# Kernel optimization log

Hardware: AMD Instinct MI355X
Metric: run time of the kernel (lower is better)

The kernel has to match this reference:

```python
import jax, jax.numpy as jnp
import numpy as np

B, T, E, H, M2 = 8, 2048, 256, 2, 134
HD = E // H


def setup_inputs() -> dict:
    key = jax.random.key(0)
    ks = jax.random.split(key, 10)
    s = 0.02
    return {
        "X": jax.random.normal(ks[0], (B, T, E), dtype=jnp.float32),
        "Y": jax.random.uniform(ks[1], (B, M2), dtype=jnp.float32),
        "wpe": s * jax.random.normal(ks[2], (T, E), dtype=jnp.float32),
        "ln1_g": jnp.ones((E,), jnp.float32), "ln1_b": jnp.zeros((E,), jnp.float32),
        "attn_w": s * jax.random.normal(ks[3], (3 * E, E), dtype=jnp.float32),
        "attn_b": jnp.zeros((3 * E,), jnp.float32),
        "attnproj_w": s * jax.random.normal(ks[4], (E, E), dtype=jnp.float32),
        "attnproj_b": jnp.zeros((E,), jnp.float32),
        "ln2_g": jnp.ones((E,), jnp.float32), "ln2_b": jnp.zeros((E,), jnp.float32),
        "fc_w": s * jax.random.normal(ks[5], (2 * E, E), dtype=jnp.float32),
        "fc_b": jnp.zeros((2 * E,), jnp.float32),
        "mlpproj_w": s * jax.random.normal(ks[6], (E, 2 * E), dtype=jnp.float32),
        "mlpproj_b": jnp.zeros((E,), jnp.float32),
        "lnf_g": jnp.ones((E,), jnp.float32), "lnf_b": jnp.zeros((E,), jnp.float32),
        "head_w": s * jax.random.normal(ks[7], (M2, E), dtype=jnp.float32),
        "head_b": jnp.zeros((M2,), jnp.float32),
    }


def _ln(x, g, b, eps=1e-5):
    mu = x.mean(-1, keepdims=True)
    var = ((x - mu) ** 2).mean(-1, keepdims=True)
    return (x - mu) * jax.lax.rsqrt(var + eps) * g + b


def reference(X, Y, wpe, ln1_g, ln1_b, attn_w, attn_b, attnproj_w, attnproj_b,
              ln2_g, ln2_b, fc_w, fc_b, mlpproj_w, mlpproj_b, lnf_g, lnf_b,
              head_w, head_b):
    # positional ids = arange(T) -> wpe itself; cls ids = [0]*T/2 + [1]*T/2
    cls_ids = np.concatenate([np.zeros(T // 2, np.int32), np.ones(T // 2, np.int32)])
    x = X + wpe + wpe[cls_ids]                      # [B,T,E] (dropout = identity, eval)

    # single Block (n_layer=1), preceded by ReLU as in cross_mod loop
    x = jax.nn.relu(x)
    h = _ln(x, ln1_g, ln1_b)
    qkv = h @ attn_w.T + attn_b                     # [B,T,3E]
    q, k, v = jnp.split(qkv, 3, axis=-1)
    q, k, v = jax.nn.relu(q), jax.nn.relu(k), jax.nn.relu(v)
    split_heads = lambda t: t.reshape(B, T, H, HD).transpose(0, 2, 1, 3)
    q, k, v = split_heads(q), split_heads(k), split_heads(v)
    att = jnp.einsum('bhqd,bhkd->bhqk', q, k) * (1.0 / np.sqrt(HD))
    tril = jnp.tril(jnp.ones((T, T), dtype=bool))
    # masked_fill(-inf) then ReLU  ==  zero outside causal mask, ReLU inside
    att = jnp.where(tril, jax.nn.relu(att), 0.0)    # [B,H,T,T]
    y = jnp.einsum('bhqk,bhkd->bhqd', att, v)
    y = y.transpose(0, 2, 1, 3).reshape(B, T, E)
    x = x + (y @ attnproj_w.T + attnproj_b)

    h = _ln(x, ln2_g, ln2_b)
    x = x + (jax.nn.relu(h @ fc_w.T + fc_b) @ mlpproj_w.T + mlpproj_b)

    x = jax.nn.relu(x)
    x = _ln(x, lnf_g, lnf_b)
    x = jax.nn.relu(x)
    emb = x.mean(axis=1)                            # [B,E]
    logits = jax.nn.relu(emb @ head_w.T + head_b)   # [B,M2]

    loss1 = jnp.sqrt(jnp.mean((logits - Y) ** 2))
    e1, e2 = emb[:, : E // 2], emb[:, E // 2:]
    loss3 = jnp.sqrt(jnp.mean((e1 - e2) ** 2))
    loss = 50.0 * loss1 + loss3
    return (e1, e2, loss, loss1, loss3, logits)
```

## Files before the change

kernel.cpp:

```cpp
#include <hip/hip_runtime.h>
#include <hip/hip_bf16.h>

#define Bc 8
#define Tc 2048
#define Ec 256
#define Hc 2
#define HDc 128
#define Mrows (Bc*Tc)
#define M2c 134

using bfx8  = __attribute__((ext_vector_type(8))) __bf16;
using f32x4 = __attribute__((ext_vector_type(4))) float;

__device__ __forceinline__ void gll16(const __bf16* g, __bf16* lds) {
    __builtin_amdgcn_global_load_lds(
        (const __attribute__((address_space(1))) unsigned int*)g,
        (__attribute__((address_space(3))) unsigned int*)lds, 16, 0, 0);
}

__global__ __launch_bounds__(256) void embed_prep_k(const float* X, const float* wpe,
                                                    const float* g, const float* bb,
                                                    const float* attn_w, const float* apw,
                                                    const float* fcw, const float* mpw,
                                                    __bf16* wb, float* embsum,
                                                    __bf16* xres, __bf16* hb) {
    int m = blockIdx.x;
    int e = threadIdx.x;
    if (m < 2048) {
        int i = m * 256 + e;
        if (i < 196608)       wb[i] = (__bf16)attn_w[i];
        else if (i < 262144)  wb[i] = (__bf16)apw[i - 196608];
        else if (i < 393216)  wb[i] = (__bf16)fcw[i - 262144];
        else                  wb[i] = (__bf16)mpw[i - 393216];
        if (m < 8) embsum[m * 256 + e] = 0.f;
    }
    int t = m & (Tc - 1);
    float v = X[(size_t)m * Ec + e] + wpe[(size_t)t * Ec + e] + wpe[(size_t)(t >= 1024) * Ec + e];
    v = fmaxf(v, 0.f);
    xres[(size_t)m * Ec + e] = (__bf16)v;
    float s1 = v, s2 = v * v;
    #pragma unroll
    for (int o = 32; o; o >>= 1) { s1 += __shfl_xor(s1, o, 64); s2 += __shfl_xor(s2, o, 64); }
    __shared__ float a1[4], a2[4];
    int w = threadIdx.x >> 6;
    if ((threadIdx.x & 63) == 0) { a1[w] = s1; a2[w] = s2; }
    __syncthreads();
    float m1 = (a1[0] + a1[1] + a1[2] + a1[3]) * (1.f / 256.f);
    float m2 = (a2[0] + a2[1] + a2[2] + a2[3]) * (1.f / 256.f);
    float r = rsqrtf(m2 - m1 * m1 + 1e-5f);
    hb[(size_t)m * Ec + e] = (__bf16)((v - m1) * r * g[e] + bb[e]);
}

__global__ __launch_bounds__(256) void gemm_qkv(const __bf16* __restrict__ A,
                                                const __bf16* __restrict__ Bw,
                                                const float* __restrict__ bias,
                                                __bf16* __restrict__ Qb,
                                                __bf16* __restrict__ Kb,
                                                __bf16* __restrict__ Vb) {
    const int K = 256;
    __shared__ __bf16 As[128 * 64];
    __shared__ __bf16 Bs[128 * 64];
    const int tid = threadIdx.x, w = tid >> 6, l = tid & 63;
    const int m0 = blockIdx.y * 128, n0 = blockIdx.x * 128;
    const int wr = w >> 1, wc = w & 1;
    const int quad = l >> 4, col15 = l & 15;

    f32x4 acc[4][4];
    f32x4 zz = {0.f, 0.f, 0.f, 0.f};
    #pragma unroll
    for (int i = 0; i < 4; i++)
        #pragma unroll
        for (int j = 0; j < 4; j++) acc[i][j] = zz;

    const int lrow = l >> 3;
    const int pbs  = l & 7;

    for (int kb = 0; kb < K; kb += 64) {
        #pragma unroll
        for (int it = 0; it < 4; it++) {
            int chunk = w * 4 + it;
            int row = chunk * 8 + lrow;
            int lb = pbs ^ (row & 7);
            gll16(A  + (size_t)(m0 + row) * K + kb + lb * 8, As + chunk * 512);
            gll16(Bw + (size_t)(n0 + row) * K + kb + lb * 8, Bs + chunk * 512);
        }
        __syncthreads();
        #pragma unroll
        for (int ks = 0; ks < 2; ks++) {
            bfx8 af[4], bfr[4];
            #pragma unroll
            for (int rt = 0; rt < 4; rt++) {
                int row = wr * 64 + rt * 16 + col15;
                int pb = (ks * 4 + quad) ^ (row & 7);
                af[rt] = *(const bfx8*)(As + row * 64 + pb * 8);
            }
            #pragma unroll
            for (int ct = 0; ct < 4; ct++) {
                int row = wc * 64 + ct * 16 + col15;
                int pb = (ks * 4 + quad) ^ (row & 7);
                bfr[ct] = *(const bfx8*)(Bs + row * 64 + pb * 8);
            }
            #pragma unroll
            for (int rt = 0; rt < 4; rt++)
                #pragma unroll
                for (int ct = 0; ct < 4; ct++)
                    acc[rt][ct] = __builtin_amdgcn_mfma_f32_16x16x32_bf16(af[rt], bfr[ct], acc[rt][ct], 0, 0, 0);
        }
        __syncthreads();
    }

    #pragma unroll
    for (int rt = 0; rt < 4; rt++)
        #pragma unroll
        for (int ct = 0; ct < 4; ct++) {
            int mgb = m0 + wr * 64 + rt * 16 + quad * 4;
            int ng  = n0 + wc * 64 + ct * 16 + col15;
            float bsv = bias[ng];
            #pragma unroll
            for (int r = 0; r < 4; r++) {
                float val = fmaxf(acc[rt][ct][r] + bsv, 0.f);
                int mg = mgb + r;
                int sel = ng >> 8;
                int hh = (ng >> 7) & 1;
                int d = ng & 127;
                int bb = mg >> 11, tt = mg & (Tc - 1);
                size_t idx = ((size_t)((bb * 2 + hh) * Tc + tt)) * HDc + d;
                __bf16 bv = (__bf16)val;
                if (sel == 0) Qb[idx] = bv;
                else if (sel == 1) Kb[idx] = bv;
                else Vb[idx] = bv;
            }
        }
}

__global__ __launch_bounds__(256) void transpose_v(const unsigned short* Vb, unsigned short* Vt) {
    __shared__ unsigned short tile[64][66];
    int kt = blockIdx.x, dt = blockIdx.y, bh = blockIdx.z;
    int tid = threadIdx.x;
    int k0 = kt * 64, d0 = dt * 64;
    int rr = tid >> 4, cc = (tid & 15) * 4;
    #pragma unroll
    for (int p = 0; p < 4; p++) {
        int k = p * 16 + rr;
        const unsigned short* src = Vb + ((size_t)(bh * Tc + k0 + k)) * HDc + d0 + cc;
        ushort4 vv = *(const ushort4*)src;
        tile[k][cc] = vv.x; tile[k][cc + 1] = vv.y; tile[k][cc + 2] = vv.z; tile[k][cc + 3] = vv.w;
    }
    __syncthreads();
    #pragma unroll
    for (int p = 0; p < 4; p++) {
        int d = p * 16 + rr;
        unsigned short* dst = Vt + ((size_t)(bh * HDc + d0 + d)) * Tc + k0 + cc;
        ushort4 ov;
        ov.x = tile[cc][d]; ov.y = tile[cc + 1][d]; ov.z = tile[cc + 2][d]; ov.w = tile[cc + 3][d];
        *(ushort4*)dst = ov;
    }
}

__global__ __launch_bounds__(256, 4) void attn6_k(const __bf16* __restrict__ Qb,
                                                  const __bf16* __restrict__ Kb,
                                                  const __bf16* __restrict__ Vt,
                                                  __bf16* __restrict__ Y1,
                                                  __bf16* __restrict__ Y2,
                                                  __bf16* __restrict__ Y3,
                                                  __bf16* __restrict__ Y4) {
    __shared__ __bf16 Ks[64 * 128];
    __shared__ __bf16 Vs[128 * 64];
    __shared__ __bf16 Ss[64 * 64];
    int bid = blockIdx.x;
    int lane8 = bid & 7;
    int s = bid >> 3;
    int bh = ((s & 1) << 3) | lane8;
    int f = s >> 1;
    int qt, ch;
    if (f < 8)       { qt = f;                    ch = 0; }
    else if (f < 24) { qt = 8 + ((f - 8) >> 1);   ch = (f - 8) & 1; }
    else if (f < 48) { int r = f - 24; int d3 = r / 3; qt = 16 + d3; ch = r - 3 * d3; }
    else             { int r = f - 48; qt = 24 + (r >> 2); ch = r & 3; }
    int Q0 = qt * 64;
    int kts = ch * 8;
    int kte = min(kts + 8, qt + 1);

    int tid = threadIdx.x, w = tid >> 6, l = tid & 63;
    int quad = l >> 4, col15 = l & 15;
    const int lrowK = l >> 4, pbsK = l & 15;
    const int lrowV = l >> 3, pbsV = l & 7;

    #pragma unroll
    for (int it = 0; it < 4; it++) {
        int chunk = w * 4 + it;
        int row = chunk * 4 + lrowK;
        int lb = pbsK ^ (row & 7);
        gll16(Qb + ((size_t)(bh * Tc + Q0 + row)) * HDc + lb * 8, Ks + chunk * 512);
    }
    __syncthreads();
    bfx8 qf[4];
    #pragma unroll
    for (int ks = 0; ks < 4; ks++) {
        int row = w * 16 + col15;
        int pb = (ks * 4 + quad) ^ (row & 7);
        qf[ks] = *(const bfx8*)(Ks + row * 128 + pb * 8);
    }

    f32x4 zz = {0.f, 0.f, 0.f, 0.f};
    f32x4 yacc[8];
    #pragma unroll
    for (int i = 0; i < 8; i++) yacc[i] = zz;

    for (int kt = kts; kt < kte; kt++) {
        __syncthreads();
        #pragma unroll
        for (int it = 0; it < 4; it++) {
            int chunk = w * 4 + it;
            int rowK = chunk * 4 + lrowK;
            int lbK = pbsK ^ (rowK & 7);
            gll16(Kb + ((size_t)(bh * Tc + kt * 64 + rowK)) * HDc + lbK * 8, Ks + chunk * 512);
            int rowV = chunk * 8 + lrowV;
            int lbV = pbsV ^ (rowV & 7);
            gll16(Vt + ((size_t)(bh * HDc + rowV)) * Tc + kt * 64 + lbV * 8, Vs + chunk * 512);
        }
        __syncthreads();

        f32x4 sacc[4];
        #pragma unroll
        for (int i = 0; i < 4; i++) sacc[i] = zz;
        #pragma unroll
        for (int ks = 0; ks < 4; ks++) {
            #pragma unroll
            for (int ct = 0; ct < 4; ct++) {
                int row = ct * 16 + col15;
                int pb = (ks * 4 + quad) ^ (row & 7);
                bfx8 kf = *(const bfx8*)(Ks + row * 128 + pb * 8);
                sacc[ct] = __builtin_amdgcn_mfma_f32_16x16x32_bf16(qf[ks], kf, sacc[ct], 0, 0, 0);
            }
        }

        #pragma unroll
        for (int ct = 0; ct < 4; ct++) {
            int kl = ct * 16 + col15;
            int kg = kt * 64 + kl;
            int blk = kl >> 3, off = kl & 7;
            #pragma unroll
            for (int r = 0; r < 4; r++) {
                int qlw = w * 16 + quad * 4 + r;
                float val = (kg <= Q0 + qlw) ? fmaxf(sacc[ct][r], 0.f) : 0.f;
                int pb = blk ^ (qlw & 7);
                Ss[qlw * 64 + pb * 8 + off] = (__bf16)val;
            }
        }

        #pragma unroll
        for (int ks = 0; ks < 2; ks++) {
            int rowS = w * 16 + col15;
            int pbS = (ks * 4 + quad) ^ (rowS & 7);
            bfx8 sf = *(const bfx8*)(Ss + rowS * 64 + pbS * 8);
            #pragma unroll
            for (int dt = 0; dt < 8; dt++) {
                int row = dt * 16 + col15;
                int pb = (ks * 4 + quad) ^ (row & 7);
                bfx8 vf = *(const bfx8*)(Vs + row * 64 + pb * 8);
                yacc[dt] = __builtin_amdgcn_mfma_f32_16x16x32_bf16(sf, vf, yacc[dt], 0, 0, 0);
            }
        }
    }

    __bf16* Yp = (ch == 0) ? Y1 : (ch == 1) ? Y2 : (ch == 2) ? Y3 : Y4;
    int b = bh >> 1, h = bh & 1;
    const float sc = 0.08838834764831845f;
    #pragma unroll
    for (int dt = 0; dt < 8; dt++) {
        int d = dt * 16 + col15;
        #pragma unroll
        for (int r = 0; r < 4; r++) {
            int q = Q0 + w * 16 + quad * 4 + r;
            Yp[((size_t)(b * Tc + q)) * Ec + h * HDc + d] = (__bf16)(yacc[dt][r] * sc);
        }
    }
}

__global__ __launch_bounds__(256, 1) void mega_k(const __bf16* __restrict__ Y1,
                                                 const __bf16* __restrict__ Y2,
                                                 const __bf16* __restrict__ Y3,
                                                 const __bf16* __restrict__ Y4,
                                                 const __bf16* __restrict__ wap,
                                                 const float* __restrict__ apb,
                                                 const __bf16* __restrict__ xres,
                                                 const float* __restrict__ ln2_g,
                                                 const float* __restrict__ ln2_b,
                                                 const __bf16* __restrict__ wfc,
                                                 const float* __restrict__ fcb,
                                                 const __bf16* __restrict__ wmp,
                                                 const float* __restrict__ mpb,
                                                 const float* __restrict__ lnf_g,
                                                 const float* __restrict__ lnf_b,
                                                 float* __restrict__ embsum) {
    __shared__ __bf16 h2s[4 * 4096];
    __shared__ __bf16 fc64[8 * 4096];
    __shared__ __bf16 Bs[256 * 64];
    __shared__ float cs[256];
    const int tid = threadIdx.x, w = tid >> 6, l = tid & 63;
    const int m0 = blockIdx.x * 64;
    const int quad = l >> 4, col15 = l & 15;
    const int lrow = l >> 3, pbs = l & 7;
    f32x4 zz = {0.f, 0.f, 0.f, 0.f};
    cs[tid] = 0.f;

    int nsum = (((m0 & (Tc - 1)) >> 6) + 8) >> 3;
    const __bf16* Ys[4] = {Y1, Y2, Y3, Y4};
    __bf16* As = fc64;

    f32x4 acc[16];
    #pragma unroll
    for (int i = 0; i < 16; i++) acc[i] = zz;

    for (int kb = 0; kb < 256; kb += 64) {
        bfx8 av[2]; int rows[2], blks[2];
        #pragma unroll
        for (int it = 0; it < 2; it++) {
            int idx = it * 256 + tid;
            int row = idx >> 3, blk = idx & 7;
            rows[it] = row; blks[it] = blk;
            size_t off = (size_t)(m0 + row) * 256 + kb + blk * 8;
            bfx8 a1 = *(const bfx8*)(Y1 + off);
            float tmp[8];
            #pragma unroll
            for (int jj = 0; jj < 8; jj++) tmp[jj] = (float)a1[jj];
            for (int j = 1; j < nsum; j++) {
                bfx8 aj = *(const bfx8*)(Ys[j] + off);
                #pragma unroll
                for (int jj = 0; jj < 8; jj++) tmp[jj] += (float)aj[jj];
            }
            #pragma unroll
            for (int jj = 0; jj < 8; jj++) a1[jj] = (__bf16)tmp[jj];
            av[it] = a1;
        }
        __syncthreads();
        #pragma unroll
        for (int it = 0; it < 2; it++) {
            int row = rows[it];
            int pb = blks[it] ^ (row & 7);
            *(bfx8*)(As + row * 64 + pb * 8) = av[it];
        }
        #pragma unroll
        for (int it = 0; it < 8; it++) {
            int chunk = w * 8 + it;
            int row = chunk * 8 + lrow;
            int lb = pbs ^ (row & 7);
            gll16(wap + (size_t)row * 256 + kb + lb * 8, Bs + chunk * 512);
        }
        __syncthreads();
        #pragma unroll
        for (int ks = 0; ks < 2; ks++) {
            int arow = w * 16 + col15;
            int apbk = (ks * 4 + quad) ^ (arow & 7);
            bfx8 af = *(const bfx8*)(As + arow * 64 + apbk * 8);
            #pragma unroll
            for (int ct = 0; ct < 16; ct++) {
                int brow = ct * 16 + col15;
                int bpb = (ks * 4 + quad) ^ (brow & 7);
                bfx8 bf = *(const bfx8*)(Bs + brow * 64 + bpb * 8);
                acc[ct] = __builtin_amdgcn_mfma_f32_16x16x32_bf16(af, bf, acc[ct], 0, 0, 0);
            }
        }
    }

    float xv[16][4];
    #pragma unroll
    for (int ct = 0; ct < 16; ct++) {
        int ng = ct * 16 + col15;
        float bsv = apb[ng];
        #pragma unroll
        for (int r = 0; r < 4; r++) {
            int mg = m0 + w * 16 + quad * 4 + r;
            xv[ct][r] = acc[ct][r] + bsv + (float)xres[(size_t)mg * 256 + ng];
        }
    }
    {
        float s1[4], s2[4];
        #pragma unroll
        for (int r = 0; r < 4; r++) {
            float a = 0.f, b2 = 0.f;
            #pragma unroll
            for (int ct = 0; ct < 16; ct++) { a += xv[ct][r]; b2 += xv[ct][r] * xv[ct][r]; }
            #pragma unroll
            for (int o = 1; o < 16; o <<= 1) { a += __shfl_xor(a, o, 64); b2 += __shfl_xor(b2, o, 64); }
            s1[r] = a; s2[r] = b2;
        }
        #pragma unroll
        for (int r = 0; r < 4; r++) {
            float mu = s1[r] * (1.f / 256.f);
            float var = s2[r] * (1.f / 256.f) - mu * mu;
            float rs = rsqrtf(var + 1e-5f);
            int row = w * 16 + quad * 4 + r;
            #pragma unroll
            for (int ct = 0; ct < 16; ct++) {
                int ng = ct * 16 + col15;
                float h = (xv[ct][r] - mu) * rs * ln2_g[ng] + ln2_b[ng];
                int panel = ng >> 6, c = ng & 63;
                h2s[panel * 4096 + row * 64 + ((c >> 3) ^ (row & 7)) * 8 + (c & 7)] = (__bf16)h;
            }
        }
    }

    for (int half = 0; half < 2; half++) {
        f32x4 acc2[16];
        #pragma unroll
        for (int i = 0; i < 16; i++) acc2[i] = zz;
        for (int kb = 0; kb < 256; kb += 64) {
            __syncthreads();
            #pragma unroll
            for (int it = 0; it < 8; it++) {
                int chunk = w * 8 + it;
                int row = chunk * 8 + lrow;
                int lb = pbs ^ (row & 7);
                gll16(wfc + (size_t)(half * 256 + row) * 256 + kb + lb * 8, Bs + chunk * 512);
            }
            __syncthreads();
            int panel = kb >> 6;
            #pragma unroll
            for (int ks = 0; ks < 2; ks++) {
                int arow = w * 16 + col15;
                int apbk = (ks * 4 + quad) ^ (arow & 7);
                bfx8 af = *(const bfx8*)(h2s + panel * 4096 + arow * 64 + apbk * 8);
                #pragma unroll
                for (int ct = 0; ct < 16; ct++) {
                    int brow = ct * 16 + col15;
                    int bpb = (ks * 4 + quad) ^ (brow & 7);
                    bfx8 bf = *(const bfx8*)(Bs + brow * 64 + bpb * 8);
                    acc2[ct] = __builtin_amdgcn_mfma_f32_16x16x32_bf16(af, bf, acc2[ct], 0, 0, 0);
                }
            }
        }
        #pragma unroll
        for (int ct = 0; ct < 16; ct++) {
            int col = half * 256 + ct * 16 + col15;
            float bsv = fcb[col];
            int panel = col >> 6, c = col & 63;
            #pragma unroll
            for (int r = 0; r < 4; r++) {
                int row = w * 16 + quad * 4 + r;
                float val = fmaxf(acc2[ct][r] + bsv, 0.f);
                fc64[panel * 4096 + row * 64 + ((c >> 3) ^ (row & 7)) * 8 + (c & 7)] = (__bf16)val;
            }
        }
    }

    #pragma unroll
    for (int i = 0; i < 16; i++) acc[i] = zz;
    for (int kb = 0; kb < 512; kb += 64) {
        __syncthreads();
        #pragma unroll
        for (int it = 0; it < 8; it++) {
            int chunk = w * 8 + it;
            int row = chunk * 8 + lrow;
            int lb = pbs ^ (row & 7);
            gll16(wmp + (size_t)row * 512 + kb + lb * 8, Bs + chunk * 512);
        }
        __syncthreads();
        int panel = kb >> 6;
        #pragma unroll
        for (int ks = 0; ks < 2; ks++) {
            int arow = w * 16 + col15;
            int apbk = (ks * 4 + quad) ^ (arow & 7);
            bfx8 af = *(const bfx8*)(fc64 + panel * 4096 + arow * 64 + apbk * 8);
            #pragma unroll
            for (int ct = 0; ct < 16; ct++) {
                int brow = ct * 16 + col15;
                int bpb = (ks * 4 + quad) ^ (brow & 7);
                bfx8 bf = *(const bfx8*)(Bs + brow * 64 + bpb * 8);
                acc[ct] = __builtin_amdgcn_mfma_f32_16x16x32_bf16(af, bf, acc[ct], 0, 0, 0);
            }
        }
    }

    #pragma unroll
    for (int ct = 0; ct < 16; ct++) {
        int ng = ct * 16 + col15;
        float bsv = mpb[ng];
        #pragma unroll
        for (int r = 0; r < 4; r++)
            xv[ct][r] = fmaxf(acc[ct][r] + bsv + xv[ct][r], 0.f);
    }
    float s1[4], s2[4];
    #pragma unroll
    for (int r = 0; r < 4; r++) {
        float a = 0.f, b2 = 0.f;
        #pragma unroll
        for (int ct = 0; ct < 16; ct++) { a += xv[ct][r]; b2 += xv[ct][r] * xv[ct][r]; }
        #pragma unroll
        for (int o = 1; o < 16; o <<= 1) { a += __shfl_xor(a, o, 64); b2 += __shfl_xor(b2, o, 64); }
        s1[r] = a; s2[r] = b2;
    }
    float colsum[16];
    #pragma unroll
    for (int ct = 0; ct < 16; ct++) colsum[ct] = 0.f;
    #pragma unroll
    for (int r = 0; r < 4; r++) {
        float mu = s1[r] * (1.f / 256.f);
        float var = s2[r] * (1.f / 256.f) - mu * mu;
        float rs = rsqrtf(var + 1e-5f);
        #pragma unroll
        for (int ct = 0; ct < 16; ct++) {
            int ng = ct * 16 + col15;
            float h = (xv[ct][r] - mu) * rs * lnf_g[ng] + lnf_b[ng];
            colsum[ct] += fmaxf(h, 0.f);
        }
    }
    #pragma unroll
    for (int ct = 0; ct < 16; ct++) {
        colsum[ct] += __shfl_xor(colsum[ct], 16, 64);
        colsum[ct] += __shfl_xor(colsum[ct], 32, 64);
    }
    if (quad == 0) {
        #pragma unroll
        for (int ct = 0; ct < 16; ct++)
            atomicAdd(&cs[ct * 16 + col15], colsum[ct]);
    }
    __syncthreads();
    atomicAdd(&embsum[(m0 >> 11) * 256 + tid], cs[tid]);
}

__global__ __launch_bounds__(256) void final_k(const float* embsum, const float* Yt,
                                               const float* head_w, const float* head_b,
                                               float* out) {
    __shared__ float semb[2048];
    __shared__ float slog[1072];
    int tid = threadIdx.x;
    for (int i = tid; i < 2048; i += 256) semb[i] = embsum[i] * (1.f / 2048.f);
    __syncthreads();
    float part1 = 0.f;
    for (int idx = tid; idx < 1072; idx += 256) {
        int b = idx / M2c, n = idx - b * M2c;
        float acc = head_b[n];
        const float* wn = head_w + (size_t)n * Ec;
        const float* e = semb + b * Ec;
        #pragma unroll 8
        for (int k = 0; k < Ec; k++) acc += e[k] * wn[k];
        acc = fmaxf(acc, 0.f);
        slog[idx] = acc;
        float d = acc - Yt[idx];
        part1 += d * d;
    }
    float part3 = 0.f;
    for (int idx = tid; idx < 1024; idx += 256) {
        int b = idx >> 7, i = idx & 127;
        float d = semb[b * Ec + i] - semb[b * Ec + 128 + i];
        part3 += d * d;
    }
    #pragma unroll
    for (int o = 32; o; o >>= 1) { part1 += __shfl_xor(part1, o, 64); part3 += __shfl_xor(part3, o, 64); }
    __shared__ float r1[4], r3[4];
    int w = tid >> 6;
    if ((tid & 63) == 0) { r1[w] = part1; r3[w] = part3; }
    __syncthreads();
    float l1 = sqrtf((r1[0] + r1[1] + r1[2] + r1[3]) / 1072.f);
    float l3 = sqrtf((r3[0] + r3[1] + r3[2] + r3[3]) / 1024.f);
    for (int idx = tid; idx < 1024; idx += 256) {
        int b = idx >> 7, i = idx & 127;
        out[idx]        = semb[b * Ec + i];
        out[1024 + idx] = semb[b * Ec + 128 + i];
    }
    if (tid == 0) {
        out[2048] = 50.f * l1 + l3;
        out[2049] = l1;
        out[2050] = l3;
    }
    for (int idx = tid; idx < 1072; idx += 256) out[2051 + idx] = slog[idx];
}

extern "C" void kernel_launch(void* const* d_in, const int* in_sizes, int n_in,
                              void* d_out, int out_size, void* d_ws, size_t ws_size,
                              hipStream_t stream) {
    const float* X        = (const float*)d_in[0];
    const float* Yt       = (const float*)d_in[1];
    const float* wpe      = (const float*)d_in[2];
    const float* ln1_g    = (const float*)d_in[3];
    const float* ln1_b    = (const float*)d_in[4];
    const float* attn_w   = (const float*)d_in[5];
    const float* attn_b   = (const float*)d_in[6];
    const float* apw      = (const float*)d_in[7];
    const float* apb      = (const float*)d_in[8];
    const float* ln2_g    = (const float*)d_in[9];
    const float* ln2_b    = (const float*)d_in[10];
    const float* fcw      = (const float*)d_in[11];
    const float* fcb      = (const float*)d_in[12];
    const float* mpw      = (const float*)d_in[13];
    const float* mpb      = (const float*)d_in[14];
    const float* lnf_g    = (const float*)d_in[15];
    const float* lnf_b    = (const float*)d_in[16];
    const float* head_w   = (const float*)d_in[17];
    const float* head_b   = (const float*)d_in[18];

    char* ws = (char*)d_ws;
    const size_t MB = 1048576;
    __bf16* xres   = (__bf16*)(ws + 0 * MB);
    __bf16* hb     = (__bf16*)(ws + 8 * MB);
    __bf16* Qb     = (__bf16*)(ws + 16 * MB);
    __bf16* Kb     = (__bf16*)(ws + 24 * MB);
    __bf16* Vb     = (__bf16*)(ws + 32 * MB);
    __bf16* Vt     = (__bf16*)(ws + 40 * MB);
    __bf16* Y1     = (__bf16*)(ws + 48 * MB);
    __bf16* Y2     = (__bf16*)(ws + 56 * MB);
    __bf16* wb     = (__bf16*)(ws + 64 * MB);
    float*  embsum = (float*)(ws + 65 * MB);

    __bf16* Y3 = hb;
    __bf16* Y4 = Vb;

    __bf16* wqkv = wb;
    __bf16* wap  = wb + 196608;
    __bf16* wfc  = wb + 262144;
    __bf16* wmp  = wb + 393216;

    embed_prep_k<<<Mrows, 256, 0, stream>>>(X, wpe, ln1_g, ln1_b,
                                            attn_w, apw, fcw, mpw, wb, embsum, xres, hb);
    gemm_qkv<<<dim3(6, 128), 256, 0, stream>>>(hb, wqkv, attn_b, Qb, Kb, Vb);
    transpose_v<<<dim3(32, 2, 16), 256, 0, stream>>>((const unsigned short*)Vb, (unsigned short*)Vt);
    attn6_k<<<1280, 256, 0, stream>>>(Qb, Kb, Vt, Y1, Y2, Y3, Y4);
    mega_k<<<256, 256, 0, stream>>>(Y1, Y2, Y3, Y4, wap, apb, xres, ln2_g, ln2_b,
                                    wfc, fcb, wmp, mpb, lnf_g, lnf_b, embsum);
    final_k<<<1, 256, 0, stream>>>(embsum, Yt, head_w, head_b, (float*)d_out);
}
```

Baseline: 250.4 us.

## Fuse V transpose into QKV GEMM epilogue and retile MLP mega kernel

The QKV GEMM now writes V tiles straight into the transposed Vt layout through an LDS staging buffer, so the separate transpose_v kernel and its extra round trip through global memory go away. The fused post-attention kernel is retiled from 64 to 32 rows per block, doubling the grid to 512 blocks with two blocks per CU. Each wave now owns a column slice of the output, reads weight fragments directly from global/L2 instead of staging them in LDS, and combines LayerNorm statistics across waves through shared memory. This trades LDS weight reuse for more parallelism, and it raises LDS use in the GEMM plus the number of global weight reads.

```diff
diff --git a/kernel.cpp b/kernel.cpp
--- a/kernel.cpp
+++ b/kernel.cpp
@@ -56,14 +56,16 @@
                                                 const float* __restrict__ bias,
                                                 __bf16* __restrict__ Qb,
                                                 __bf16* __restrict__ Kb,
-                                                __bf16* __restrict__ Vb) {
+                                                unsigned short* __restrict__ Vt) {
     const int K = 256;
     __shared__ __bf16 As[128 * 64];
     __shared__ __bf16 Bs[128 * 64];
+    __shared__ unsigned short trans[128][136];
     const int tid = threadIdx.x, w = tid >> 6, l = tid & 63;
     const int m0 = blockIdx.y * 128, n0 = blockIdx.x * 128;
     const int wr = w >> 1, wc = w & 1;
     const int quad = l >> 4, col15 = l & 15;
+    const int isV = (n0 >= 512);
 
     f32x4 acc[4][4];
     f32x4 zz = {0.f, 0.f, 0.f, 0.f};
@@ -113,47 +115,39 @@
     for (int rt = 0; rt < 4; rt++)
         #pragma unroll
         for (int ct = 0; ct < 4; ct++) {
-            int mgb = m0 + wr * 64 + rt * 16 + quad * 4;
             int ng  = n0 + wc * 64 + ct * 16 + col15;
             float bsv = bias[ng];
             #pragma unroll
             for (int r = 0; r < 4; r++) {
+                int mg = m0 + wr * 64 + rt * 16 + quad * 4 + r;
                 float val = fmaxf(acc[rt][ct][r] + bsv, 0.f);
-                int mg = mgb + r;
-                int sel = ng >> 8;
-                int hh = (ng >> 7) & 1;
-                int d = ng & 127;
-                int bb = mg >> 11, tt = mg & (Tc - 1);
-                size_t idx = ((size_t)((bb * 2 + hh) * Tc + tt)) * HDc + d;
                 __bf16 bv = (__bf16)val;
-                if (sel == 0) Qb[idx] = bv;
-                else if (sel == 1) Kb[idx] = bv;
-                else Vb[idx] = bv;
-            }
-        }
-}
-
-__global__ __launch_bounds__(256) void transpose_v(const unsigned short* Vb, unsigned short* Vt) {
-    __shared__ unsigned short tile[64][66];
-    int kt = blockIdx.x, dt = blockIdx.y, bh = blockIdx.z;
-    int tid = threadIdx.x;
-    int k0 = kt * 64, d0 = dt * 64;
-    int rr = tid >> 4, cc = (tid & 15) * 4;
-    #pragma unroll
-    for (int p = 0; p < 4; p++) {
-        int k = p * 16 + rr;
-        const unsigned short* src = Vb + ((size_t)(bh * Tc + k0 + k)) * HDc + d0 + cc;
-        ushort4 vv = *(const ushort4*)src;
-        tile[k][cc] = vv.x; tile[k][cc + 1] = vv.y; tile[k][cc + 2] = vv.z; tile[k][cc + 3] = vv.w;
-    }
-    __syncthreads();
-    #pragma unroll
-    for (int p = 0; p < 4; p++) {
-        int d = p * 16 + rr;
-        unsigned short* dst = Vt + ((size_t)(bh * HDc + d0 + d)) * Tc + k0 + cc;
-        ushort4 ov;
-        ov.x = tile[cc][d]; ov.y = tile[cc + 1][d]; ov.z = tile[cc + 2][d]; ov.w = tile[cc + 3][d];
-        *(ushort4*)dst = ov;
+                if (isV) {
+                    int d = ng & 127;
+                    int tl = mg - m0;
+                    trans[d][tl] = *(unsigned short*)&bv;
+                } else {
+                    int sel = ng >> 8;
+                    int hh = (ng >> 7) & 1;
+                    int d = ng & 127;
+                    int bb = mg >> 11, tt = mg & (Tc - 1);
+                    size_t idx = ((size_t)((bb * 2 + hh) * Tc + tt)) * HDc + d;
+                    if (sel == 0) Qb[idx] = bv;
+                    else Kb[idx] = bv;
+                }
+            }
+        }
+    if (isV) {
+        __syncthreads();
+        int h = (n0 >> 7) & 1;
+        int b = m0 >> 11, t0 = m0 & (Tc - 1);
+        int bh = b * 2 + h;
+        int d = tid >> 1, th = tid & 1;
+        unsigned short* dst = Vt + ((size_t)(bh * HDc + d)) * Tc + t0 + th * 64;
+        const unsigned short* src = &trans[d][th * 64];
+        #pragma unroll
+        for (int i = 0; i < 8; i++)
+            *(uint4*)(dst + i * 8) = *(const uint4*)(src + i * 8);
     }
 }
 
@@ -278,243 +272,245 @@
     }
 }
 
-__global__ __launch_bounds__(256, 1) void mega_k(const __bf16* __restrict__ Y1,
+__global__ __launch_bounds__(256, 2) void mega_k(const __bf16* __restrict__ Y1,
                                                  const __bf16* __restrict__ Y2,
                                                  const __bf16* __restrict__ Y3,
                                                  const __bf16* __restrict__ Y4,
                                                  const __bf16* __restrict__ wap,
-                                                 const float* __restrict__ apb,
+                                                 const float* __restrict__ apbias,
                                                  const __bf16* __restrict__ xres,
                                                  const float* __restrict__ ln2_g,
                                                  const float* __restrict__ ln2_b,
                                                  const __bf16* __restrict__ wfc,
-                                                 const float* __restrict__ fcb,
+                                                 const float* __restrict__ fcbias,
                                                  const __bf16* __restrict__ wmp,
-                                                 const float* __restrict__ mpb,
+                                                 const float* __restrict__ mpbias,
                                                  const float* __restrict__ lnf_g,
                                                  const float* __restrict__ lnf_b,
                                                  float* __restrict__ embsum) {
-    __shared__ __bf16 h2s[4 * 4096];
-    __shared__ __bf16 fc64[8 * 4096];
-    __shared__ __bf16 Bs[256 * 64];
+    __shared__ __bf16 fcs[32 * 512];
+    __shared__ __bf16 h2s[32 * 256];
+    __shared__ float red1[32][4], red2[32][4];
     __shared__ float cs[256];
+    __bf16* As = fcs;
+
     const int tid = threadIdx.x, w = tid >> 6, l = tid & 63;
-    const int m0 = blockIdx.x * 64;
+    const int m0 = blockIdx.x * 32;
     const int quad = l >> 4, col15 = l & 15;
-    const int lrow = l >> 3, pbs = l & 7;
     f32x4 zz = {0.f, 0.f, 0.f, 0.f};
-    cs[tid] = 0.f;
-
-    int nsum = (((m0 & (Tc - 1)) >> 6) + 8) >> 3;
+
+    int qt = (m0 & (Tc - 1)) >> 6;
+    int nsum = (qt + 8) >> 3;
     const __bf16* Ys[4] = {Y1, Y2, Y3, Y4};
-    __bf16* As = fc64;
-
-    f32x4 acc[16];
-    #pragma unroll
-    for (int i = 0; i < 16; i++) acc[i] = zz;
-
-    for (int kb = 0; kb < 256; kb += 64) {
-        bfx8 av[2]; int rows[2], blks[2];
-        #pragma unroll
-        for (int it = 0; it < 2; it++) {
-            int idx = it * 256 + tid;
-            int row = idx >> 3, blk = idx & 7;
-            rows[it] = row; blks[it] = blk;
-            size_t off = (size_t)(m0 + row) * 256 + kb + blk * 8;
-            bfx8 a1 = *(const bfx8*)(Y1 + off);
-            float tmp[8];
-            #pragma unroll
-            for (int jj = 0; jj < 8; jj++) tmp[jj] = (float)a1[jj];
-            for (int j = 1; j < nsum; j++) {
-                bfx8 aj = *(const bfx8*)(Ys[j] + off);
-                #pragma unroll
-                for (int jj = 0; jj < 8; jj++) tmp[jj] += (float)aj[jj];
-            }
-            #pragma unroll
-            for (int jj = 0; jj < 8; jj++) a1[jj] = (__bf16)tmp[jj];
-            av[it] = a1;
-        }
-        __syncthreads();
-        #pragma unroll
-        for (int it = 0; it < 2; it++) {
-            int row = rows[it];
-            int pb = blks[it] ^ (row & 7);
-            *(bfx8*)(As + row * 64 + pb * 8) = av[it];
-        }
-        #pragma unroll
-        for (int it = 0; it < 8; it++) {
-            int chunk = w * 8 + it;
-            int row = chunk * 8 + lrow;
-            int lb = pbs ^ (row & 7);
-            gll16(wap + (size_t)row * 256 + kb + lb * 8, Bs + chunk * 512);
-        }
-        __syncthreads();
-        #pragma unroll
-        for (int ks = 0; ks < 2; ks++) {
-            int arow = w * 16 + col15;
-            int apbk = (ks * 4 + quad) ^ (arow & 7);
-            bfx8 af = *(const bfx8*)(As + arow * 64 + apbk * 8);
-            #pragma unroll
-            for (int ct = 0; ct < 16; ct++) {
-                int brow = ct * 16 + col15;
-                int bpb = (ks * 4 + quad) ^ (brow & 7);
-                bfx8 bf = *(const bfx8*)(Bs + brow * 64 + bpb * 8);
-                acc[ct] = __builtin_amdgcn_mfma_f32_16x16x32_bf16(af, bf, acc[ct], 0, 0, 0);
-            }
-        }
-    }
-
-    float xv[16][4];
-    #pragma unroll
-    for (int ct = 0; ct < 16; ct++) {
-        int ng = ct * 16 + col15;
-        float bsv = apb[ng];
-        #pragma unroll
-        for (int r = 0; r < 4; r++) {
-            int mg = m0 + w * 16 + quad * 4 + r;
-            xv[ct][r] = acc[ct][r] + bsv + (float)xres[(size_t)mg * 256 + ng];
-        }
-    }
-    {
-        float s1[4], s2[4];
+
+    #pragma unroll
+    for (int it = 0; it < 4; it++) {
+        int idx = it * 256 + tid;
+        int row = idx >> 5, blk = idx & 31;
+        size_t off = (size_t)(m0 + row) * 256 + blk * 8;
+        bfx8 a1 = *(const bfx8*)(Y1 + off);
+        float tmp[8];
+        #pragma unroll
+        for (int jj = 0; jj < 8; jj++) tmp[jj] = (float)a1[jj];
+        for (int j = 1; j < nsum; j++) {
+            bfx8 aj = *(const bfx8*)(Ys[j] + off);
+            #pragma unroll
+            for (int jj = 0; jj < 8; jj++) tmp[jj] += (float)aj[jj];
+        }
+        #pragma unroll
+        for (int jj = 0; jj < 8; jj++) a1[jj] = (__bf16)tmp[jj];
+        *(bfx8*)(As + row * 256 + (blk ^ (row & 7)) * 8) = a1;
+    }
+    __syncthreads();
+
+    f32x4 acc1[2][4];
+    #pragma unroll
+    for (int rt = 0; rt < 2; rt++)
+        #pragma unroll
+        for (int ct = 0; ct < 4; ct++) acc1[rt][ct] = zz;
+    #pragma unroll
+    for (int kw = 0; kw < 8; kw++) {
+        bfx8 af[2], bf[4];
+        #pragma unroll
+        for (int rt = 0; rt < 2; rt++) {
+            int row = rt * 16 + col15;
+            int pb = (kw * 4 + quad) ^ (row & 7);
+            af[rt] = *(const bfx8*)(As + row * 256 + pb * 8);
+        }
+        #pragma unroll
+        for (int ct = 0; ct < 4; ct++)
+            bf[ct] = *(const bfx8*)(wap + (size_t)(w * 64 + ct * 16 + col15) * 256 + kw * 32 + quad * 8);
+        #pragma unroll
+        for (int rt = 0; rt < 2; rt++)
+            #pragma unroll
+            for (int ct = 0; ct < 4; ct++)
+                acc1[rt][ct] = __builtin_amdgcn_mfma_f32_16x16x32_bf16(af[rt], bf[ct], acc1[rt][ct], 0, 0, 0);
+    }
+
+    float xv[2][4][4];
+    #pragma unroll
+    for (int rt = 0; rt < 2; rt++)
+        #pragma unroll
+        for (int ct = 0; ct < 4; ct++) {
+            int ng = w * 64 + ct * 16 + col15;
+            float bsv = apbias[ng];
+            #pragma unroll
+            for (int r = 0; r < 4; r++) {
+                int mg = m0 + rt * 16 + quad * 4 + r;
+                xv[rt][ct][r] = acc1[rt][ct][r] + bsv + (float)xres[(size_t)mg * 256 + ng];
+            }
+        }
+    #pragma unroll
+    for (int rt = 0; rt < 2; rt++)
         #pragma unroll
         for (int r = 0; r < 4; r++) {
             float a = 0.f, b2 = 0.f;
             #pragma unroll
-            for (int ct = 0; ct < 16; ct++) { a += xv[ct][r]; b2 += xv[ct][r] * xv[ct][r]; }
+            for (int ct = 0; ct < 4; ct++) { a += xv[rt][ct][r]; b2 += xv[rt][ct][r] * xv[rt][ct][r]; }
             #pragma unroll
             for (int o = 1; o < 16; o <<= 1) { a += __shfl_xor(a, o, 64); b2 += __shfl_xor(b2, o, 64); }
-            s1[r] = a; s2[r] = b2;
-        }
+            if (col15 == 0) {
+                int row = rt * 16 + quad * 4 + r;
+                red1[row][w] = a; red2[row][w] = b2;
+            }
+        }
+    __syncthreads();
+    #pragma unroll
+    for (int rt = 0; rt < 2; rt++)
         #pragma unroll
         for (int r = 0; r < 4; r++) {
-            float mu = s1[r] * (1.f / 256.f);
-            float var = s2[r] * (1.f / 256.f) - mu * mu;
+            int row = rt * 16 + quad * 4 + r;
+            float s1 = red1[row][0] + red1[row][1] + red1[row][2] + red1[row][3];
+            float s2 = red2[row][0] + red2[row][1] + red2[row][2] + red2[row][3];
+            float mu = s1 * (1.f / 256.f);
+            float var = s2 * (1.f / 256.f) - mu * mu;
             float rs = rsqrtf(var + 1e-5f);
-            int row = w * 16 + quad * 4 + r;
-            #pragma unroll
-            for (int ct = 0; ct < 16; ct++) {
-                int ng = ct * 16 + col15;
-                float h = (xv[ct][r] - mu) * rs * ln2_g[ng] + ln2_b[ng];
-                int panel = ng >> 6, c = ng & 63;
-                h2s[panel * 4096 + row * 64 + ((c >> 3) ^ (row & 7)) * 8 + (c & 7)] = (__bf16)h;
-            }
-        }
-    }
-
-    for (int half = 0; half < 2; half++) {
-        f32x4 acc2[16];
-        #pragma unroll
-        for (int i = 0; i < 16; i++) acc2[i] = zz;
-        for (int kb = 0; kb < 256; kb += 64) {
-            __syncthreads();
-            #pragma unroll
-            for (int it = 0; it < 8; it++) {
-                int chunk = w * 8 + it;
-                int row = chunk * 8 + lrow;
-                int lb = pbs ^ (row & 7);
-                gll16(wfc + (size_t)(half * 256 + row) * 256 + kb + lb * 8, Bs + chunk * 512);
-            }
-            __syncthreads();
-            int panel = kb >> 6;
-            #pragma unroll
-            for (int ks = 0; ks < 2; ks++) {
-                int arow = w * 16 + col15;
-                int apbk = (ks * 4 + quad) ^ (arow & 7);
-                bfx8 af = *(const bfx8*)(h2s + panel * 4096 + arow * 64 + apbk * 8);
+            #pragma unroll
+            for (int ct = 0; ct < 4; ct++) {
+                int ng = w * 64 + ct * 16 + col15;
+                float h = (xv[rt][ct][r] - mu) * rs * ln2_g[ng] + ln2_b[ng];
+                h2s[row * 256 + ((ng >> 3) ^ (row & 7)) * 8 + (ng & 7)] = (__bf16)h;
+            }
+        }
+    __syncthreads();
+
+    for (int g2 = 0; g2 < 2; g2++) {
+        f32x4 acc2[2][4];
+        #pragma unroll
+        for (int rt = 0; rt < 2; rt++)
+            #pragma unroll
+            for (int ct = 0; ct < 4; ct++) acc2[rt][ct] = zz;
+        #pragma unroll
+        for (int kw = 0; kw < 8; kw++) {
+            bfx8 af[2], bf[4];
+            #pragma unroll
+            for (int rt = 0; rt < 2; rt++) {
+                int row = rt * 16 + col15;
+                int pb = (kw * 4 + quad) ^ (row & 7);
+                af[rt] = *(const bfx8*)(h2s + row * 256 + pb * 8);
+            }
+            #pragma unroll
+            for (int ct = 0; ct < 4; ct++)
+                bf[ct] = *(const bfx8*)(wfc + (size_t)(w * 128 + g2 * 64 + ct * 16 + col15) * 256 + kw * 32 + quad * 8);
+            #pragma unroll
+            for (int rt = 0; rt < 2; rt++)
                 #pragma unroll
-                for (int ct = 0; ct < 16; ct++) {
-                    int brow = ct * 16 + col15;
-                    int bpb = (ks * 4 + quad) ^ (brow & 7);
-                    bfx8 bf = *(const bfx8*)(Bs + brow * 64 + bpb * 8);
-                    acc2[ct] = __builtin_amdgcn_mfma_f32_16x16x32_bf16(af, bf, acc2[ct], 0, 0, 0);
+                for (int ct = 0; ct < 4; ct++)
+                    acc2[rt][ct] = __builtin_amdgcn_mfma_f32_16x16x32_bf16(af[rt], bf[ct], acc2[rt][ct], 0, 0, 0);
+        }
+        #pragma unroll
+        for (int rt = 0; rt < 2; rt++)
+            #pragma unroll
+            for (int ct = 0; ct < 4; ct++) {
+                int col = w * 128 + g2 * 64 + ct * 16 + col15;
+                float bsv = fcbias[col];
+                #pragma unroll
+                for (int r = 0; r < 4; r++) {
+                    int row = rt * 16 + quad * 4 + r;
+                    float val = fmaxf(acc2[rt][ct][r] + bsv, 0.f);
+                    fcs[row * 512 + ((col >> 3) ^ (row & 7)) * 8 + (col & 7)] = (__bf16)val;
                 }
             }
-        }
-        #pragma unroll
-        for (int ct = 0; ct < 16; ct++) {
-            int col = half * 256 + ct * 16 + col15;
-            float bsv = fcb[col];
-            int panel = col >> 6, c = col & 63;
-            #pragma unroll
-            for (int r = 0; r < 4; r++) {
-                int row = w * 16 + quad * 4 + r;
-                float val = fmaxf(acc2[ct][r] + bsv, 0.f);
-                fc64[panel * 4096 + row * 64 + ((c >> 3) ^ (row & 7)) * 8 + (c & 7)] = (__bf16)val;
-            }
-        }
-    }
-
-    #pragma unroll
-    for (int i = 0; i < 16; i++) acc[i] = zz;
-    for (int kb = 0; kb < 512; kb += 64) {
-        __syncthreads();
-        #pragma unroll
-        for (int it = 0; it < 8; it++) {
-            int chunk = w * 8 + it;
-            int row = chunk * 8 + lrow;
-            int lb = pbs ^ (row & 7);
-            gll16(wmp + (size_t)row * 512 + kb + lb * 8, Bs + chunk * 512);
-        }
-        __syncthreads();
-        int panel = kb >> 6;
-        #pragma unroll
-        for (int ks = 0; ks < 2; ks++) {
-            int arow = w * 16 + col15;
-            int apbk = (ks * 4 + quad) ^ (arow & 7);
-            bfx8 af = *(const bfx8*)(fc64 + panel * 4096 + arow * 64 + apbk * 8);
-            #pragma unroll
-            for (int ct = 0; ct < 16; ct++) {
-                int brow = ct * 16 + col15;
-                int bpb = (ks * 4 + quad) ^ (brow & 7);
-                bfx8 bf = *(const bfx8*)(Bs + brow * 64 + bpb * 8);
-                acc[ct] = __builtin_amdgcn_mfma_f32_16x16x32_bf16(af, bf, acc[ct], 0, 0, 0);
-            }
-        }
-    }
-
-    #pragma unroll
-    for (int ct = 0; ct < 16; ct++) {
-        int ng = ct * 16 + col15;
-        float bsv = mpb[ng];
-        #pragma unroll
-        for (int r = 0; r < 4; r++)
-            xv[ct][r] = fmaxf(acc[ct][r] + bsv + xv[ct][r], 0.f);
-    }
-    float s1[4], s2[4];
-    #pragma unroll
-    for (int r = 0; r < 4; r++) {
-        float a = 0.f, b2 = 0.f;
-        #pragma unroll
-        for (int ct = 0; ct < 16; ct++) { a += xv[ct][r]; b2 += xv[ct][r] * xv[ct][r]; }
-        #pragma unroll
-        for (int o = 1; o < 16; o <<= 1) { a += __shfl_xor(a, o, 64); b2 += __shfl_xor(b2, o, 64); }
-        s1[r] = a; s2[r] = b2;
-    }
-    float colsum[16];
-    #pragma unroll
-    for (int ct = 0; ct < 16; ct++) colsum[ct] = 0.f;
-    #pragma unroll
-    for (int r = 0; r < 4; r++) {
-        float mu = s1[r] * (1.f / 256.f);
-        float var = s2[r] * (1.f / 256.f) - mu * mu;
-        float rs = rsqrtf(var + 1e-5f);
-        #pragma unroll
-        for (int ct = 0; ct < 16; ct++) {
-            int ng = ct * 16 + col15;
-            float h = (xv[ct][r] - mu) * rs * lnf_g[ng] + lnf_b[ng];
-            colsum[ct] += fmaxf(h, 0.f);
-        }
-    }
-    #pragma unroll
-    for (int ct = 0; ct < 16; ct++) {
+    }
+    __syncthreads();
+
+    f32x4 acc3[2][4];
+    #pragma unroll
+    for (int rt = 0; rt < 2; rt++)
+        #pragma unroll
+        for (int ct = 0; ct < 4; ct++) acc3[rt][ct] = zz;
+    #pragma unroll
+    for (int kw = 0; kw < 16; kw++) {
+        bfx8 af[2], bf[4];
+        #pragma unroll
+        for (int rt = 0; rt < 2; rt++) {
+            int row = rt * 16 + col15;
+            int pb = (kw * 4 + quad) ^ (row & 7);
+            af[rt] = *(const bfx8*)(fcs + row * 512 + pb * 8);
+        }
+        #pragma unroll
+        for (int ct = 0; ct < 4; ct++)
+            bf[ct] = *(const bfx8*)(wmp + (size_t)(w * 64 + ct * 16 + col15) * 512 + kw * 32 + quad * 8);
+        #pragma unroll
+        for (int rt = 0; rt < 2; rt++)
+            #pragma unroll
+            for (int ct = 0; ct < 4; ct++)
+                acc3[rt][ct] = __builtin_amdgcn_mfma_f32_16x16x32_bf16(af[rt], bf[ct], acc3[rt][ct], 0, 0, 0);
+    }
+
+    #pragma unroll
+    for (int rt = 0; rt < 2; rt++)
+        #pragma unroll
+        for (int ct = 0; ct < 4; ct++) {
+            int ng = w * 64 + ct * 16 + col15;
+            float bsv = mpbias[ng];
+            #pragma unroll
+            for (int r = 0; r < 4; r++)
+                xv[rt][ct][r] = fmaxf(acc3[rt][ct][r] + bsv + xv[rt][ct][r], 0.f);
+        }
+    __syncthreads();
+    #pragma unroll
+    for (int rt = 0; rt < 2; rt++)
+        #pragma unroll
+        for (int r = 0; r < 4; r++) {
+            float a = 0.f, b2 = 0.f;
+            #pragma unroll
+            for (int ct = 0; ct < 4; ct++) { a += xv[rt][ct][r]; b2 += xv[rt][ct][r] * xv[rt][ct][r]; }
+            #pragma unroll
+            for (int o = 1; o < 16; o <<= 1) { a += __shfl_xor(a, o, 64); b2 += __shfl_xor(b2, o, 64); }
+            if (col15 == 0) {
+                int row = rt * 16 + quad * 4 + r;
+                red1[row][w] = a; red2[row][w] = b2;
+            }
+        }
+    __syncthreads();
+    float colsum[4] = {0.f, 0.f, 0.f, 0.f};
+    #pragma unroll
+    for (int rt = 0; rt < 2; rt++)
+        #pragma unroll
+        for (int r = 0; r < 4; r++) {
+            int row = rt * 16 + quad * 4 + r;
+            float s1 = red1[row][0] + red1[row][1] + red1[row][2] + red1[row][3];
+            float s2 = red2[row][0] + red2[row][1] + red2[row][2] + red2[row][3];
+            float mu = s1 * (1.f / 256.f);
+            float var = s2 * (1.f / 256.f) - mu * mu;
+            float rs = rsqrtf(var + 1e-5f);
+            #pragma unroll
+            for (int ct = 0; ct < 4; ct++) {
+                int ng = w * 64 + ct * 16 + col15;
+                float h = (xv[rt][ct][r] - mu) * rs * lnf_g[ng] + lnf_b[ng];
+                colsum[ct] += fmaxf(h, 0.f);
+            }
+        }
+    #pragma unroll
+    for (int ct = 0; ct < 4; ct++) {
         colsum[ct] += __shfl_xor(colsum[ct], 16, 64);
         colsum[ct] += __shfl_xor(colsum[ct], 32, 64);
     }
     if (quad == 0) {
         #pragma unroll
-        for (int ct = 0; ct < 16; ct++)
-            atomicAdd(&cs[ct * 16 + col15], colsum[ct]);
+        for (int ct = 0; ct < 4; ct++)
+            cs[w * 64 + ct * 16 + col15] = colsum[ct];
     }
     __syncthreads();
     atomicAdd(&embsum[(m0 >> 11) * 256 + tid], cs[tid]);
@@ -614,10 +610,9 @@
 
     embed_prep_k<<<Mrows, 256, 0, stream>>>(X, wpe, ln1_g, ln1_b,
                                             attn_w, apw, fcw, mpw, wb, embsum, xres, hb);
-    gemm_qkv<<<dim3(6, 128), 256, 0, stream>>>(hb, wqkv, attn_b, Qb, Kb, Vb);
-    transpose_v<<<dim3(32, 2, 16), 256, 0, stream>>>((const unsigned short*)Vb, (unsigned short*)Vt);
+    gemm_qkv<<<dim3(6, 128), 256, 0, stream>>>(hb, wqkv, attn_b, Qb, Kb, (unsigned short*)Vt);
     attn6_k<<<1280, 256, 0, stream>>>(Qb, Kb, Vt, Y1, Y2, Y3, Y4);
-    mega_k<<<256, 256, 0, stream>>>(Y1, Y2, Y3, Y4, wap, apb, xres, ln2_g, ln2_b,
+    mega_k<<<512, 256, 0, stream>>>(Y1, Y2, Y3, Y4, wap, apb, xres, ln2_g, ln2_b,
                                     wfc, fcb, wmp, mpb, lnf_g, lnf_b, embsum);
     final_k<<<1, 256, 0, stream>>>(embsum, Yt, head_w, head_b, (float*)d_out);
 }
```

Result: no change. 252.9 us (+1.0%).
